# Optimization experiments

Measured on AMD Instinct MI355X. Metric: run time of the kernel, lower is better.

The kernel has to match this reference:

```python
import jax, jax.numpy as jnp
import numpy as np

EMB = 1024
NH = 16
T = 2048
B = 2

def setup_inputs() -> dict:
    key = jax.random.key(0)
    k1, k2, k3, k4, k5 = jax.random.split(key, 5)
    s = 0.02
    return {
        "x": jax.random.normal(k1, (B, T, EMB), dtype=jnp.float32),
        "W_attn": jax.random.normal(k2, (EMB, 3 * EMB), dtype=jnp.float32) * s,
        "b_attn": jax.random.normal(k3, (3 * EMB,), dtype=jnp.float32) * s,
        "W_proj": jax.random.normal(k4, (EMB, EMB), dtype=jnp.float32) * s,
        "b_proj": jax.random.normal(k5, (EMB,), dtype=jnp.float32) * s,
    }

def reference(x, W_attn, b_attn, W_proj, b_proj):
    Bz, Tz, C = x.shape
    hd = C // NH
    qkv = x @ W_attn + b_attn                      # [B,T,3C]
    q, k, v = jnp.split(qkv, 3, axis=-1)
    # [B,T,C] -> [B,H,T,hd]
    def heads(t):
        return t.reshape(Bz, Tz, NH, hd).transpose(0, 2, 1, 3)
    q, k, v = heads(q), heads(k), heads(v)
    scale = 1.0 / jnp.sqrt(jnp.float32(hd))
    att = jnp.einsum("bhqd,bhkd->bhqk", q, k) * scale   # [B,H,T,T]
    causal = jnp.tril(jnp.ones((Tz, Tz), dtype=bool))
    att = jnp.where(causal, att, jnp.finfo(att.dtype).min)
    att = jax.nn.softmax(att, axis=-1)
    y = jnp.einsum("bhqk,bhkd->bhqd", att, v)            # [B,H,T,hd]
    y = y.transpose(0, 2, 1, 3).reshape(Bz, Tz, C)
    return y @ W_proj + b_proj
```

## Files before the change

kernel.cpp:

```cpp
#include <hip/hip_runtime.h>
#include <cstdint>
#include <cstddef>

typedef _Float16 half8 __attribute__((ext_vector_type(8)));
typedef _Float16 half4v __attribute__((ext_vector_type(4)));
typedef float f32x4 __attribute__((ext_vector_type(4)));
typedef int int4v __attribute__((ext_vector_type(4)));

#define EMBD 1024
#define NHEAD 16
#define TSEQ 2048
#define NB 2
#define HD 64
#define NBH (NB*NHEAD)
#define SCK 0.18033688f

static __device__ __forceinline__ void gload_lds16(const void* g, void* l) {
    __builtin_amdgcn_global_load_lds((const __attribute__((address_space(1))) void*)g,
                                     (__attribute__((address_space(3))) void*)l,
                                     16, 0, 0);
}

static __device__ __forceinline__ int pk2(float a, float b) {
    return __builtin_bit_cast(int, __builtin_amdgcn_cvt_pkrtz(a, b));
}

__global__ __launch_bounds__(256) void k_prep(
    const float* __restrict__ x,  _Float16* __restrict__ xh,
    const float* __restrict__ Wa, const float* __restrict__ Wp,
    _Float16* __restrict__ WaT,   _Float16* __restrict__ WpT)
{
    const int bx = blockIdx.x;
    if (bx < 4096) {
        int i = bx * 256 + threadIdx.x;
        float4 v = ((const float4*)x)[i];
        half4v h;
        h.x = (_Float16)v.x; h.y = (_Float16)v.y; h.z = (_Float16)v.z; h.w = (_Float16)v.w;
        ((half4v*)xh)[i] = h;
        return;
    }
    __shared__ float tile[32][33];
    const int idx = bx - 4096;
    const int bxx = idx & 127;
    const int byy = idx >> 7;
    const bool isA = bxx < 96;
    const float* in  = isA ? Wa : Wp;
    _Float16* out    = isA ? WaT : WpT;
    const int C      = isA ? 3072 : 1024;
    const int c0 = (isA ? bxx : bxx - 96) * 32, r0 = byy * 32;
    const int tx = threadIdx.x & 31, ty = threadIdx.x >> 5;
    #pragma unroll
    for (int j = 0; j < 4; ++j)
        tile[ty + 8*j][tx] = in[(size_t)(r0 + ty + 8*j) * C + c0 + tx];
    __syncthreads();
    #pragma unroll
    for (int j = 0; j < 4; ++j)
        out[(size_t)(c0 + ty + 8*j) * 1024 + r0 + tx] = (_Float16)tile[tx][ty + 8*j];
}

__global__ __launch_bounds__(256) void k_gemm_qkv(
    const _Float16* __restrict__ A,
    const _Float16* __restrict__ Bt,
    const float* __restrict__ bias,
    _Float16* __restrict__ outq,
    _Float16* __restrict__ VT)
{
    __shared__ _Float16 smem[20480];
    _Float16* As = smem;

    const int d   = blockIdx.x;
    const int xcd = d & 7;
    const int idx = d >> 3;
    const int mt  = (xcd >> 1) * 8 + (idx & 7);
    const int ntl = (xcd &  1) * 8 + (idx >> 3);
    const int m0 = mt * 128;
    const int hc = ntl * 64;

    const int tid  = threadIdx.x;
    const int lane = tid & 63;
    const int w    = tid >> 6;
    const int wm   = w >> 1, wn = w & 1;
    const int l15  = lane & 15;
    const int lg   = lane >> 4;

    f32x4 acc[3][4][2];
    #pragma unroll
    for (int q = 0; q < 3; ++q)
        #pragma unroll
        for (int i = 0; i < 4; ++i) {
            acc[q][i][0] = (f32x4){0.f, 0.f, 0.f, 0.f};
            acc[q][i][1] = (f32x4){0.f, 0.f, 0.f, 0.f};
        }

    for (int kt = 0; kt < 16; ++kt) {
        __syncthreads();
        #pragma unroll
        for (int c = 0; c < 4; ++c) {
            int s = c * 256 + tid;
            int r = s >> 3, sl = s & 7;
            const _Float16* ga = A + (size_t)(m0 + r) * 1024 + kt * 64 + ((sl ^ (r & 7)) * 8);
            gload_lds16(ga, (char*)As + s * 16);
        }
        #pragma unroll
        for (int q = 0; q < 3; ++q) {
            #pragma unroll
            for (int c = 0; c < 2; ++c) {
                int s = c * 256 + tid;
                int r = s >> 3, sl = s & 7;
                const _Float16* gb = Bt + (size_t)(q * 1024 + hc + r) * 1024 + kt * 64 + ((sl ^ (r & 7)) * 8);
                gload_lds16(gb, (char*)(smem + 8192 + q * 4096) + s * 16);
            }
        }
        __syncthreads();

        half8 af[4][2];
        #pragma unroll
        for (int mf = 0; mf < 4; ++mf) {
            int r = wm * 64 + mf * 16 + l15;
            #pragma unroll
            for (int ks = 0; ks < 2; ++ks)
                af[mf][ks] = *(const half8*)((const char*)As + r * 128 + (((ks * 4 + lg) ^ (r & 7)) * 16));
        }
        #pragma unroll
        for (int q = 0; q < 3; ++q) {
            const char* BsQ = (const char*)(smem + 8192 + q * 4096);
            half8 bf[2][2];
            #pragma unroll
            for (int nf = 0; nf < 2; ++nf) {
                int r = wn * 32 + nf * 16 + l15;
                #pragma unroll
                for (int ks = 0; ks < 2; ++ks)
                    bf[nf][ks] = *(const half8*)(BsQ + r * 128 + (((ks * 4 + lg) ^ (r & 7)) * 16));
            }
            #pragma unroll
            for (int mf = 0; mf < 4; ++mf)
                #pragma unroll
                for (int nf = 0; nf < 2; ++nf) {
                    acc[q][mf][nf] = __builtin_amdgcn_mfma_f32_16x16x32_f16(af[mf][0], bf[nf][0], acc[q][mf][nf], 0, 0, 0);
                    acc[q][mf][nf] = __builtin_amdgcn_mfma_f32_16x16x32_f16(af[mf][1], bf[nf][1], acc[q][mf][nf], 0, 0, 0);
                }
        }
    }

    #pragma unroll
    for (int q = 0; q < 2; ++q) {
        float bv0 = bias[q * 1024 + hc + wn * 32 + l15];
        float bv1 = bias[q * 1024 + hc + wn * 32 + 16 + l15];
        const float osc = (q == 1) ? SCK : 1.0f;
        #pragma unroll
        for (int mf = 0; mf < 4; ++mf) {
            #pragma unroll
            for (int j = 0; j < 4; ++j) {
                int m = m0 + wm * 64 + mf * 16 + lg * 4 + j;
                _Float16* po = outq + (size_t)m * 3072 + q * 1024 + hc + wn * 32 + l15;
                po[0]  = (_Float16)((acc[q][mf][0][j] + bv0) * osc);
                po[16] = (_Float16)((acc[q][mf][1][j] + bv1) * osc);
            }
        }
    }
    {
        float bv0 = bias[2048 + hc + wn * 32 + l15];
        float bv1 = bias[2048 + hc + wn * 32 + 16 + l15];
        __syncthreads();
        #pragma unroll
        for (int mf = 0; mf < 4; ++mf)
            #pragma unroll
            for (int j = 0; j < 4; ++j) {
                int m = wm * 64 + mf * 16 + lg * 4 + j;
                smem[m * 65 + wn * 32 + l15]      = (_Float16)(acc[2][mf][0][j] + bv0);
                smem[m * 65 + wn * 32 + 16 + l15] = (_Float16)(acc[2][mf][1][j] + bv1);
            }
        __syncthreads();

        const int b     = m0 >> 11;
        const int tloc0 = m0 & 2047;
        _Float16* vbase = VT + ((size_t)(b * 16 + ntl) * 64) * 2048 + tloc0;
        #pragma unroll
        for (int c = 0; c < 4; ++c) {
            int seg = c * 256 + tid;
            int dd  = seg >> 4;
            int s   = seg & 15;
            half8 hv8;
            #pragma unroll
            for (int e = 0; e < 8; ++e) {
                int p = s * 8 + e;
                int k = 16 * (2 * (p >> 5) + ((p & 7) >> 2)) + 4 * ((p >> 3) & 3) + (p & 3);
                hv8[e] = smem[k * 65 + dd];
            }
            *(half8*)&vbase[(size_t)dd * 2048 + s * 8] = hv8;
        }
    }
}

__global__ __launch_bounds__(256) void k_gemm_proj(
    const _Float16* __restrict__ A,
    const _Float16* __restrict__ Bt,
    const float* __restrict__ bias,
    float* __restrict__ outf)
{
    __shared__ _Float16 As[64 * 64];
    __shared__ _Float16 Bs[128 * 64];

    const int d   = blockIdx.x;
    const int xcd = d & 7;
    const int idx = d >> 3;
    const int mt  = (xcd >> 1) * 16 + (idx & 15);
    const int nt  = (xcd &  1) * 4  + (idx >> 4);
    const int m0 = mt * 64, n0 = nt * 128;

    const int tid  = threadIdx.x;
    const int lane = tid & 63;
    const int wn   = tid >> 6;
    const int l15  = lane & 15;
    const int lg   = lane >> 4;

    f32x4 acc[4][2];
    #pragma unroll
    for (int i = 0; i < 4; ++i) {
        acc[i][0] = (f32x4){0.f, 0.f, 0.f, 0.f};
        acc[i][1] = (f32x4){0.f, 0.f, 0.f, 0.f};
    }

    for (int kt = 0; kt < 16; ++kt) {
        __syncthreads();
        #pragma unroll
        for (int c = 0; c < 2; ++c) {
            int s = c * 256 + tid;
            int r = s >> 3, sl = s & 7;
            const _Float16* ga = A + (size_t)(m0 + r) * 1024 + kt * 64 + ((sl ^ (r & 7)) * 8);
            gload_lds16(ga, (char*)As + s * 16);
        }
        #pragma unroll
        for (int c = 0; c < 4; ++c) {
            int s = c * 256 + tid;
            int r = s >> 3, sl = s & 7;
            const _Float16* gb = Bt + (size_t)(n0 + r) * 1024 + kt * 64 + ((sl ^ (r & 7)) * 8);
            gload_lds16(gb, (char*)Bs + s * 16);
        }
        __syncthreads();

        half8 af[4][2], bf[2][2];
        #pragma unroll
        for (int mf = 0; mf < 4; ++mf) {
            int r = mf * 16 + l15;
            #pragma unroll
            for (int ks = 0; ks < 2; ++ks)
                af[mf][ks] = *(const half8*)((const char*)As + r * 128 + (((ks * 4 + lg) ^ (r & 7)) * 16));
        }
        #pragma unroll
        for (int nf = 0; nf < 2; ++nf) {
            int r = wn * 32 + nf * 16 + l15;
            #pragma unroll
            for (int ks = 0; ks < 2; ++ks)
                bf[nf][ks] = *(const half8*)((const char*)Bs + r * 128 + (((ks * 4 + lg) ^ (r & 7)) * 16));
        }
        #pragma unroll
        for (int mf = 0; mf < 4; ++mf)
            #pragma unroll
            for (int nf = 0; nf < 2; ++nf) {
                acc[mf][nf] = __builtin_amdgcn_mfma_f32_16x16x32_f16(af[mf][0], bf[nf][0], acc[mf][nf], 0, 0, 0);
                acc[mf][nf] = __builtin_amdgcn_mfma_f32_16x16x32_f16(af[mf][1], bf[nf][1], acc[mf][nf], 0, 0, 0);
            }
    }

    float bv[2];
    bv[0] = bias[n0 + wn * 32 + l15];
    bv[1] = bias[n0 + wn * 32 + 16 + l15];

    #pragma unroll
    for (int mf = 0; mf < 4; ++mf) {
        #pragma unroll
        for (int j = 0; j < 4; ++j) {
            int m = m0 + mf * 16 + lg * 4 + j;
            float* po = outf + (size_t)m * 1024 + n0 + wn * 32 + l15;
            po[0]  = acc[mf][0][j] + bv[0];
            po[16] = acc[mf][1][j] + bv[1];
        }
    }
}

__global__ __launch_bounds__(512) void k_attn(
    const _Float16* __restrict__ qkv,
    const _Float16* __restrict__ VTg,
    _Float16* __restrict__ Y)
{
    __shared__ _Float16 Kt[2][8192];
    __shared__ _Float16 Vt[2][8192];

    const int tid  = threadIdx.x;
    const int lane = tid & 63;
    const int w    = tid >> 6;
    const int l15  = lane & 15;
    const int lg   = lane >> 4;
    const int bh   = blockIdx.x;
    const int by   = blockIdx.y;
    const int qt   = (by < 8) ? (15 - by) : (by - 8);
    const int b    = bh >> 4, h = bh & 15;

    const int rA  = tid >> 3;
    const int slA = tid & 7;
    const size_t kOffA = (size_t)rA * 3072 + ((slA ^ (rA & 7)) * 8);
    const _Float16* kBase = qkv + (size_t)(b * 2048) * 3072 + 1024 + h * 64;

    const int dA = tid >> 4;
    const int sA = tid & 15;
    const size_t vOffA = (size_t)dA * 2048 + ((sA ^ (dA & 15)) * 8);
    const _Float16* vBase = VTg + (size_t)bh * TSEQ * HD;

    const int x7   = l15 & 7;
    const int kph0 = (lg ^ x7) * 8;
    const int kph1 = ((4 + lg) ^ x7) * 8;

    const int qrow = qt * 128 + w * 16 + l15;
    const _Float16* qptr = qkv + (size_t)(b * 2048 + qrow) * 3072 + h * 64;
    half8 qa0 = *(const half8*)&qptr[lg * 8];
    half8 qa1 = *(const half8*)&qptr[32 + lg * 8];

    half8 ones;
    #pragma unroll
    for (int i = 0; i < 8; ++i) ones[i] = (_Float16)1.0f;

    f32x4 yac[4];
    #pragma unroll
    for (int nf = 0; nf < 4; ++nf) yac[nf] = (f32x4){0.f, 0.f, 0.f, 0.f};
    f32x4 lsum = (f32x4){0.f, 0.f, 0.f, 0.f};

    const int nkt = qt + 1;

    half8 kra = *(const half8*)(kBase + kOffA);
    half8 krb = *(const half8*)(kBase + kOffA + (size_t)64 * 3072);
    half8 vra = *(const half8*)(vBase + vOffA);
    half8 vrb = *(const half8*)(vBase + vOffA + 32 * 2048);

    for (int kt = 0; kt < nkt; ++kt) {
        const int cur = kt & 1;
        _Float16* KtC = Kt[cur];
        _Float16* VtC = Vt[cur];
        *(half8*)&KtC[tid * 8]        = kra;
        *(half8*)&KtC[4096 + tid * 8] = krb;
        *(half8*)&VtC[tid * 8]        = vra;
        *(half8*)&VtC[4096 + tid * 8] = vrb;
        if (kt + 1 < nkt) {
            const _Float16* kp = kBase + (size_t)(kt + 1) * 128 * 3072;
            kra = *(const half8*)(kp + kOffA);
            krb = *(const half8*)(kp + kOffA + (size_t)64 * 3072);
            const _Float16* vp = vBase + (kt + 1) * 128;
            vra = *(const half8*)(vp + vOffA);
            vrb = *(const half8*)(vp + vOffA + 32 * 2048);
        }
        asm volatile("s_waitcnt lgkmcnt(0)" ::: "memory");
        __builtin_amdgcn_s_barrier();
        __builtin_amdgcn_sched_barrier(0);

        const bool diag = (kt == nkt - 1);

        f32x4 s[8];
        __builtin_amdgcn_s_setprio(1);
        #pragma unroll
        for (int f = 0; f < 8; ++f) {
            if (diag && f > w) { s[f] = (f32x4){0.f, 0.f, 0.f, 0.f}; continue; }
            int rr = f * 16 + l15;
            half8 kb0 = *(const half8*)&KtC[rr * 64 + kph0];
            half8 kb1 = *(const half8*)&KtC[rr * 64 + kph1];
            f32x4 z = (f32x4){0.f, 0.f, 0.f, 0.f};
            z = __builtin_amdgcn_mfma_f32_16x16x32_f16(kb0, qa0, z, 0, 0, 0);
            z = __builtin_amdgcn_mfma_f32_16x16x32_f16(kb1, qa1, z, 0, 0, 0);
            s[f] = z;
        }
        __builtin_amdgcn_s_setprio(0);

        if (diag) {
            const int qg = qt * 128 + w * 16 + l15;
            #pragma unroll
            for (int f = 0; f < 8; ++f) {
                if (f > w) continue;
                #pragma unroll
                for (int j = 0; j < 4; ++j) {
                    int kk = kt * 128 + 16 * f + 4 * lg + j;
                    s[f][j] = (kk > qg) ? 0.f : exp2f(s[f][j]);
                }
            }
        } else {
            #pragma unroll
            for (int f = 0; f < 8; ++f)
                #pragma unroll
                for (int j = 0; j < 4; ++j) s[f][j] = exp2f(s[f][j]);
        }

        __builtin_amdgcn_s_setprio(1);
        #pragma unroll
        for (int t = 0; t < 4; ++t) {
            int4v pi;
            pi[0] = pk2(s[2 * t][0],     s[2 * t][1]);
            pi[1] = pk2(s[2 * t][2],     s[2 * t][3]);
            pi[2] = pk2(s[2 * t + 1][0], s[2 * t + 1][1]);
            pi[3] = pk2(s[2 * t + 1][2], s[2 * t + 1][3]);
            half8 pa = __builtin_bit_cast(half8, pi);
            lsum = __builtin_amdgcn_mfma_f32_16x16x32_f16(pa, ones, lsum, 0, 0, 0);
            #pragma unroll
            for (int nf = 0; nf < 4; ++nf) {
                half8 vb = *(const half8*)&VtC[(nf * 16 + l15) * 128 + (((t * 4 + lg) ^ l15) * 8)];
                yac[nf] = __builtin_amdgcn_mfma_f32_16x16x32_f16(pa, vb, yac[nf], 0, 0, 0);
            }
        }
        __builtin_amdgcn_s_setprio(0);
    }

    const int trow = qt * 128 + w * 16 + lg * 4;
    #pragma unroll
    for (int j = 0; j < 4; ++j) {
        float inv = 1.f / lsum[j];
        #pragma unroll
        for (int nf = 0; nf < 4; ++nf) {
            float yv = yac[nf][j] * inv;
            Y[((size_t)b * TSEQ + trow + j) * EMBD + h * 64 + nf * 16 + l15] = (_Float16)yv;
        }
    }
}

extern "C" void kernel_launch(void* const* d_in, const int* in_sizes, int n_in,
                              void* d_out, int out_size, void* d_ws, size_t ws_size,
                              hipStream_t stream) {
    const float* x  = (const float*)d_in[0];
    const float* Wa = (const float*)d_in[1];
    const float* ba = (const float*)d_in[2];
    const float* Wp = (const float*)d_in[3];
    const float* bp = (const float*)d_in[4];
    float* out = (float*)d_out;

    _Float16* Xh   = (_Float16*)d_ws;
    _Float16* WaT  = Xh   + (size_t)4096 * 1024;
    _Float16* WpT  = WaT  + (size_t)3072 * 1024;
    _Float16* QKVn = WpT  + (size_t)1024 * 1024;
    _Float16* VTb  = QKVn + (size_t)4096 * 3072;
    _Float16* Yh   = Xh;

    k_prep<<<8192, 256, 0, stream>>>(x, Xh, Wa, Wp, WaT, WpT);

    k_gemm_qkv<<<512, 256, 0, stream>>>(Xh, WaT, ba, QKVn, VTb);

    k_attn<<<dim3(NBH, 16), 512, 0, stream>>>(QKVn, VTb, Yh);

    k_gemm_proj<<<512, 256, 0, stream>>>(Yh, WpT, bp, out);
}
```

Before: 94.87 us.

## Use 8 waves per block in QKV GEMM with 48-column warp tiles

Raises the QKV GEMM from 256 to 512 threads per block and changes the wave layout from 2x2 to 2x4. Each wave now covers a 64x48 slice across the concatenated Q/K/V columns, so it holds 12 accumulators instead of 24. The aim is to lower register pressure and give the scheduler more waves to hide latency. The cost is more waves competing for barriers and LDS per block, plus epilogue branches where a wave's columns cross q/k/v boundaries.

```diff
diff --git a/kernel.cpp b/kernel.cpp
--- a/kernel.cpp
+++ b/kernel.cpp
@@ -58,7 +58,7 @@
         out[(size_t)(c0 + ty + 8*j) * 1024 + r0 + tx] = (_Float16)tile[tx][ty + 8*j];
 }
 
-__global__ __launch_bounds__(256) void k_gemm_qkv(
+__global__ __launch_bounds__(512, 4) void k_gemm_qkv(
     const _Float16* __restrict__ A,
     const _Float16* __restrict__ Bt,
     const float* __restrict__ bias,
@@ -79,37 +79,35 @@
     const int tid  = threadIdx.x;
     const int lane = tid & 63;
     const int w    = tid >> 6;
-    const int wm   = w >> 1, wn = w & 1;
+    const int wm   = w >> 2;
+    const int wn   = w & 3;
     const int l15  = lane & 15;
     const int lg   = lane >> 4;
 
-    f32x4 acc[3][4][2];
-    #pragma unroll
-    for (int q = 0; q < 3; ++q)
-        #pragma unroll
-        for (int i = 0; i < 4; ++i) {
-            acc[q][i][0] = (f32x4){0.f, 0.f, 0.f, 0.f};
-            acc[q][i][1] = (f32x4){0.f, 0.f, 0.f, 0.f};
-        }
+    f32x4 acc[4][3];
+    #pragma unroll
+    for (int i = 0; i < 4; ++i)
+        #pragma unroll
+        for (int j = 0; j < 3; ++j)
+            acc[i][j] = (f32x4){0.f, 0.f, 0.f, 0.f};
 
     for (int kt = 0; kt < 16; ++kt) {
         __syncthreads();
         #pragma unroll
-        for (int c = 0; c < 4; ++c) {
-            int s = c * 256 + tid;
+        for (int c = 0; c < 2; ++c) {
+            int s = c * 512 + tid;
             int r = s >> 3, sl = s & 7;
             const _Float16* ga = A + (size_t)(m0 + r) * 1024 + kt * 64 + ((sl ^ (r & 7)) * 8);
             gload_lds16(ga, (char*)As + s * 16);
         }
-        #pragma unroll
-        for (int q = 0; q < 3; ++q) {
-            #pragma unroll
-            for (int c = 0; c < 2; ++c) {
-                int s = c * 256 + tid;
-                int r = s >> 3, sl = s & 7;
-                const _Float16* gb = Bt + (size_t)(q * 1024 + hc + r) * 1024 + kt * 64 + ((sl ^ (r & 7)) * 8);
-                gload_lds16(gb, (char*)(smem + 8192 + q * 4096) + s * 16);
-            }
+        {
+            int s = tid;
+            int r = s >> 3, sl = s & 7;
+            size_t goff = (size_t)(hc + r) * 1024 + kt * 64 + ((sl ^ (r & 7)) * 8);
+            #pragma unroll
+            for (int q = 0; q < 3; ++q)
+                gload_lds16(Bt + goff + (size_t)q * 1024 * 1024,
+                            (char*)(smem + 8192 + q * 4096) + s * 16);
         }
         __syncthreads();
 
@@ -121,63 +119,69 @@
             for (int ks = 0; ks < 2; ++ks)
                 af[mf][ks] = *(const half8*)((const char*)As + r * 128 + (((ks * 4 + lg) ^ (r & 7)) * 16));
         }
-        #pragma unroll
-        for (int q = 0; q < 3; ++q) {
-            const char* BsQ = (const char*)(smem + 8192 + q * 4096);
-            half8 bf[2][2];
-            #pragma unroll
-            for (int nf = 0; nf < 2; ++nf) {
-                int r = wn * 32 + nf * 16 + l15;
+        half8 bf[3][2];
+        #pragma unroll
+        for (int nf = 0; nf < 3; ++nf) {
+            int nn = wn * 48 + nf * 16;
+            const char* BsQ = (const char*)(smem + 8192 + (nn >> 6) * 4096);
+            int r = (nn & 63) + l15;
+            #pragma unroll
+            for (int ks = 0; ks < 2; ++ks)
+                bf[nf][ks] = *(const half8*)(BsQ + r * 128 + (((ks * 4 + lg) ^ (r & 7)) * 16));
+        }
+        #pragma unroll
+        for (int mf = 0; mf < 4; ++mf)
+            #pragma unroll
+            for (int nf = 0; nf < 3; ++nf) {
+                acc[mf][nf] = __builtin_amdgcn_mfma_f32_16x16x32_f16(af[mf][0], bf[nf][0], acc[mf][nf], 0, 0, 0);
+                acc[mf][nf] = __builtin_amdgcn_mfma_f32_16x16x32_f16(af[mf][1], bf[nf][1], acc[mf][nf], 0, 0, 0);
+            }
+    }
+
+    #pragma unroll
+    for (int nf = 0; nf < 3; ++nf) {
+        int nn = wn * 48 + nf * 16;
+        int q  = nn >> 6;
+        if (q < 2) {
+            int col = (nn & 63) + l15;
+            float bv = bias[q * 1024 + hc + col];
+            float osc = (q == 1) ? SCK : 1.0f;
+            #pragma unroll
+            for (int mf = 0; mf < 4; ++mf) {
                 #pragma unroll
-                for (int ks = 0; ks < 2; ++ks)
-                    bf[nf][ks] = *(const half8*)(BsQ + r * 128 + (((ks * 4 + lg) ^ (r & 7)) * 16));
-            }
-            #pragma unroll
-            for (int mf = 0; mf < 4; ++mf)
+                for (int j = 0; j < 4; ++j) {
+                    int m = m0 + wm * 64 + mf * 16 + lg * 4 + j;
+                    outq[(size_t)m * 3072 + q * 1024 + hc + col] = (_Float16)((acc[mf][nf][j] + bv) * osc);
+                }
+            }
+        }
+    }
+    __syncthreads();
+    #pragma unroll
+    for (int nf = 0; nf < 3; ++nf) {
+        int nn = wn * 48 + nf * 16;
+        if ((nn >> 6) == 2) {
+            int col = (nn & 63) + l15;
+            float bv = bias[2048 + hc + col];
+            #pragma unroll
+            for (int mf = 0; mf < 4; ++mf) {
                 #pragma unroll
-                for (int nf = 0; nf < 2; ++nf) {
-                    acc[q][mf][nf] = __builtin_amdgcn_mfma_f32_16x16x32_f16(af[mf][0], bf[nf][0], acc[q][mf][nf], 0, 0, 0);
-                    acc[q][mf][nf] = __builtin_amdgcn_mfma_f32_16x16x32_f16(af[mf][1], bf[nf][1], acc[q][mf][nf], 0, 0, 0);
+                for (int j = 0; j < 4; ++j) {
+                    int ml = wm * 64 + mf * 16 + lg * 4 + j;
+                    smem[ml * 65 + col] = (_Float16)(acc[mf][nf][j] + bv);
                 }
-        }
-    }
-
-    #pragma unroll
-    for (int q = 0; q < 2; ++q) {
-        float bv0 = bias[q * 1024 + hc + wn * 32 + l15];
-        float bv1 = bias[q * 1024 + hc + wn * 32 + 16 + l15];
-        const float osc = (q == 1) ? SCK : 1.0f;
-        #pragma unroll
-        for (int mf = 0; mf < 4; ++mf) {
-            #pragma unroll
-            for (int j = 0; j < 4; ++j) {
-                int m = m0 + wm * 64 + mf * 16 + lg * 4 + j;
-                _Float16* po = outq + (size_t)m * 3072 + q * 1024 + hc + wn * 32 + l15;
-                po[0]  = (_Float16)((acc[q][mf][0][j] + bv0) * osc);
-                po[16] = (_Float16)((acc[q][mf][1][j] + bv1) * osc);
-            }
-        }
-    }
+            }
+        }
+    }
+    __syncthreads();
+
     {
-        float bv0 = bias[2048 + hc + wn * 32 + l15];
-        float bv1 = bias[2048 + hc + wn * 32 + 16 + l15];
-        __syncthreads();
-        #pragma unroll
-        for (int mf = 0; mf < 4; ++mf)
-            #pragma unroll
-            for (int j = 0; j < 4; ++j) {
-                int m = wm * 64 + mf * 16 + lg * 4 + j;
-                smem[m * 65 + wn * 32 + l15]      = (_Float16)(acc[2][mf][0][j] + bv0);
-                smem[m * 65 + wn * 32 + 16 + l15] = (_Float16)(acc[2][mf][1][j] + bv1);
-            }
-        __syncthreads();
-
         const int b     = m0 >> 11;
         const int tloc0 = m0 & 2047;
         _Float16* vbase = VT + ((size_t)(b * 16 + ntl) * 64) * 2048 + tloc0;
         #pragma unroll
-        for (int c = 0; c < 4; ++c) {
-            int seg = c * 256 + tid;
+        for (int c = 0; c < 2; ++c) {
+            int seg = c * 512 + tid;
             int dd  = seg >> 4;
             int s   = seg & 15;
             half8 hv8;
@@ -437,7 +441,7 @@
 
     k_prep<<<8192, 256, 0, stream>>>(x, Xh, Wa, Wp, WaT, WpT);
 
-    k_gemm_qkv<<<512, 256, 0, stream>>>(Xh, WaT, ba, QKVn, VTb);
+    k_gemm_qkv<<<512, 512, 0, stream>>>(Xh, WaT, ba, QKVn, VTb);
 
     k_attn<<<dim3(NBH, 16), 512, 0, stream>>>(QKVn, VTb, Yh);
 
```

Result: faster. 91.70 us (-3.3%).
